# Optimization experiments

Measured on AMD Instinct MI355X. Metric: run time of the kernel, lower is better.

Reference implementation:

```python
import jax, jax.numpy as jnp
import numpy as np

N_NODES = 100000
N_EDGES = 1200000
D_IN = 64
D_HID = 64


def _gcn_layer(h_in, W, b, src, dst, norm, n_nodes):
    # h_in: [N, d_in]; W: [d_in, d_out]; norm: [E_total] symmetric deg norm
    h = h_in @ W                                  # [N, d_out]
    msg = h[src] * norm[:, None]                  # gather + scale, [E_total, d_out]
    agg = jax.ops.segment_sum(msg, dst, num_segments=n_nodes)  # scatter-add
    return agg + b


def _prelu(x, a):
    # per-channel PReLU: a broadcasts over nodes
    return jnp.where(x >= 0, x, a * x)


def setup_inputs() -> dict:
    key = jax.random.key(0)
    ks = jax.random.split(key, 8)
    x = jax.random.normal(ks[0], (N_NODES, D_IN), dtype=jnp.float32)
    edge_index = jax.random.randint(ks[1], (2, N_EDGES), 0, N_NODES, dtype=jnp.int64)
    # Glorot-ish weights, PyG GCNConv defaults: weight + bias; PReLU init slope 0.25
    W1 = jax.random.normal(ks[2], (D_IN, D_HID), dtype=jnp.float32) / np.sqrt(D_IN)
    b1 = jnp.zeros((D_HID,), dtype=jnp.float32)
    a1 = jnp.full((D_HID,), 0.25, dtype=jnp.float32)
    W2 = jax.random.normal(ks[3], (D_HID, D_HID), dtype=jnp.float32) / np.sqrt(D_HID)
    b2 = jnp.zeros((D_HID,), dtype=jnp.float32)
    a2 = jnp.full((D_HID,), 0.25, dtype=jnp.float32)
    return {"x": x, "edge_index": edge_index, "W1": W1, "b1": b1, "a1": a1,
            "W2": W2, "b2": b2, "a2": a2}


def reference(x, edge_index, W1, b1, a1, W2, b2, a2):
    n = x.shape[0]
    # add self-loops (GCNConv default add_self_loops=True)
    loops = jnp.arange(n, dtype=edge_index.dtype)
    src = jnp.concatenate([edge_index[0], loops])
    dst = jnp.concatenate([edge_index[1], loops])
    # symmetric normalization: deg computed on destination with unit edge weights
    deg = jax.ops.segment_sum(jnp.ones_like(src, dtype=x.dtype), dst, num_segments=n)
    dinv = jnp.where(deg > 0, jax.lax.rsqrt(deg), 0.0)
    norm = dinv[src] * dinv[dst]                  # [E + N]

    h = _gcn_layer(x, W1, b1, src, dst, norm, n)
    h = _prelu(h, a1)
    h = _gcn_layer(h, W2, b2, src, dst, norm, n)
    h = _prelu(h, a2)
    return h
```

## Files before the change

### kernel.cpp

```cpp
#include <hip/hip_runtime.h>
#include <hip/hip_bf16.h>
#include <hip/hip_fp16.h>

#define D 64
#define NB 256
#define BSHIFT 8
#define SUBS 8
#define SCAP 1024
#define CHUNK 4096
#define AGN 32
#define BFSTRIDE 16

typedef _Float16 f16x8 __attribute__((ext_vector_type(8)));
typedef float    f32x4 __attribute__((ext_vector_type(4)));


__global__ void __launch_bounds__(256, 4)
k_bin_gemm(const int* __restrict__ src, const int* __restrict__ dst,
           unsigned* __restrict__ records, int* __restrict__ bucket_fill,
           int E, int nbin,
           const float* __restrict__ X, const float* __restrict__ W,
           __half* __restrict__ H, int n, int ntiles, int gemmb) {
    __shared__ int cnt[512];
    __shared__ int gbase[512];
    const int t = threadIdx.x;

    if ((int)blockIdx.x < nbin) {
        const int slot = blockIdx.x & (SUBS - 1);
        cnt[t] = 0; cnt[t + 256] = 0;
        __syncthreads();

        const int base_e = blockIdx.x * CHUNK;
        unsigned rec[16];
        unsigned br[16];
#pragma unroll
        for (int i = 0; i < 16; ++i) {
            int e = base_e + i * 256 + t;
            if (e < E) {
                int s = src[e], d = dst[e];
                int bk = d >> BSHIFT;
                rec[i] = ((unsigned)s << BSHIFT) | (unsigned)(d & (NB - 1));
                int rank = atomicAdd(&cnt[bk], 1);
                br[i] = ((unsigned)bk << 16) | (unsigned)rank;
            } else {
                br[i] = 0xFFFFFFFFu;
            }
        }
        __syncthreads();
#pragma unroll
        for (int rep = 0; rep < 2; ++rep) {
            int bk = t + rep * 256;
            if (cnt[bk] > 0)
                gbase[bk] = atomicAdd(&bucket_fill[(bk * SUBS + slot) * BFSTRIDE], cnt[bk]);
        }
        __syncthreads();
#pragma unroll
        for (int i = 0; i < 16; ++i) {
            if (br[i] != 0xFFFFFFFFu) {
                int bk = br[i] >> 16;
                int idx = gbase[bk] + (int)(br[i] & 0xFFFF);
                if (idx < SCAP)
                    records[((size_t)bk * SUBS + slot) * SCAP + idx] = rec[i];
            }
        }
    } else {
        const int lane = t & 63;
        const int wv   = t >> 6;
        const int r16  = lane & 15;
        const int g4   = lane >> 4;

        f16x8 Bh[4][2], Bl[4][2];
#pragma unroll
        for (int ct = 0; ct < 4; ++ct)
#pragma unroll
            for (int kt = 0; kt < 2; ++kt)
#pragma unroll
                for (int j = 0; j < 8; ++j) {
                    float w = W[(kt * 32 + g4 * 8 + j) * D + ct * 16 + r16];
                    _Float16 h = (_Float16)w;
                    Bh[ct][kt][j] = h;
                    Bl[ct][kt][j] = (_Float16)(w - (float)h);
                }

        const int gw = (blockIdx.x - nbin) * 4 + wv;
        for (int tile = gw; tile < ntiles; tile += gemmb * 4) {
            const int nb16 = tile * 16;
            int row = nb16 + r16;
            if (row > n - 1) row = n - 1;
            const float* xp = X + (size_t)row * D + g4 * 8;
            float4 x0 = *reinterpret_cast<const float4*>(xp);
            float4 x1 = *reinterpret_cast<const float4*>(xp + 4);
            float4 x2 = *reinterpret_cast<const float4*>(xp + 32);
            float4 x3 = *reinterpret_cast<const float4*>(xp + 36);
            float xs[16] = {x0.x, x0.y, x0.z, x0.w, x1.x, x1.y, x1.z, x1.w,
                            x2.x, x2.y, x2.z, x2.w, x3.x, x3.y, x3.z, x3.w};
            f16x8 Ah[2], Al[2];
#pragma unroll
            for (int kt = 0; kt < 2; ++kt)
#pragma unroll
                for (int j = 0; j < 8; ++j) {
                    float v = xs[kt * 8 + j];
                    _Float16 h = (_Float16)v;
                    Ah[kt][j] = h;
                    Al[kt][j] = (_Float16)(v - (float)h);
                }

            f32x4 acc[4];
#pragma unroll
            for (int ct = 0; ct < 4; ++ct)
                acc[ct] = (f32x4){0.f, 0.f, 0.f, 0.f};
#pragma unroll
            for (int ct = 0; ct < 4; ++ct) {
#pragma unroll
                for (int kt = 0; kt < 2; ++kt) {
                    acc[ct] = __builtin_amdgcn_mfma_f32_16x16x32_f16(Ah[kt], Bh[ct][kt], acc[ct], 0, 0, 0);
                    acc[ct] = __builtin_amdgcn_mfma_f32_16x16x32_f16(Al[kt], Bh[ct][kt], acc[ct], 0, 0, 0);
                    acc[ct] = __builtin_amdgcn_mfma_f32_16x16x32_f16(Ah[kt], Bl[ct][kt], acc[ct], 0, 0, 0);
                }
            }
#pragma unroll
            for (int ct = 0; ct < 4; ++ct)
#pragma unroll
                for (int r = 0; r < 4; ++r) {
                    int node = nb16 + g4 * 4 + r;
                    if (node < n)
                        H[(size_t)node * D + ct * 16 + r16] = __float2half_rn(acc[ct][r]);
                }
        }
    }
}


__global__ void k_csr(const unsigned* __restrict__ records,
                      const int* __restrict__ bucket_fill,
                      int* __restrict__ rowptr, float* __restrict__ dinv,
                      int* __restrict__ csr_src, __half* __restrict__ H,
                      int n, int E) {
    __shared__ int bscan[256];
    __shared__ int binc[512];
    __shared__ int cnt[NB];
    __shared__ int excl[NB];
    __shared__ float ddi[NB];
    __shared__ int stage[SUBS * SCAP];

    const int t = threadIdx.x;
    const int b = blockIdx.x;
    const int nbuckets = gridDim.x;

    int s0 = 0, s1 = 0;
#pragma unroll
    for (int s = 0; s < SUBS; ++s) {
        if (2 * t     < nbuckets) s0 += bucket_fill[((2 * t)     * SUBS + s) * BFSTRIDE];
        if (2 * t + 1 < nbuckets) s1 += bucket_fill[((2 * t + 1) * SUBS + s) * BFSTRIDE];
    }
    bscan[t] = s0 + s1;
    __syncthreads();
    for (int off = 1; off < 256; off <<= 1) {
        int val = bscan[t];
        if (t >= off) val += bscan[t - off];
        __syncthreads();
        bscan[t] = val;
        __syncthreads();
    }
    {
        int ep = bscan[t] - (s0 + s1);
        binc[2 * t]     = ep + s0;
        binc[2 * t + 1] = ep + s0 + s1;
    }
    __syncthreads();
    const int base  = (b == 0) ? 0 : binc[b - 1];
    if (b == nbuckets - 1 && t == 0) rowptr[n] = binc[nbuckets - 1];

    int subcnt[SUBS];
    int cnt_e = 0;
#pragma unroll
    for (int s = 0; s < SUBS; ++s) {
        subcnt[s] = bucket_fill[(b * SUBS + s) * BFSTRIDE];
        cnt_e += subcnt[s];
    }

    cnt[t] = 0;
    __syncthreads();
#pragma unroll
    for (int s = 0; s < SUBS; ++s) {
        const size_t so = ((size_t)b * SUBS + s) * SCAP;
        for (int i = t; i < subcnt[s]; i += 256)
            atomicAdd(&cnt[records[so + i] & (NB - 1)], 1);
    }
    __syncthreads();

    const int c0 = cnt[t];
    bscan[t] = c0;
    __syncthreads();
    for (int off = 1; off < 256; off <<= 1) {
        int val = bscan[t];
        if (t >= off) val += bscan[t - off];
        __syncthreads();
        bscan[t] = val;
        __syncthreads();
    }
    excl[t] = bscan[t] - c0;
    {
        int node = b * NB + t;
        float di = rsqrtf((float)(c0 + 1));
        ddi[t] = di;
        if (node < n) {
            rowptr[node] = base + excl[t];
            dinv[node]   = di;
        }
        cnt[t] = 0;
    }
    __syncthreads();

#pragma unroll
    for (int s = 0; s < SUBS; ++s) {
        const size_t so = ((size_t)b * SUBS + s) * SCAP;
        for (int i = t; i < subcnt[s]; i += 256) {
            unsigned r = records[so + i];
            int d8 = r & (NB - 1);
            int rank = atomicAdd(&cnt[d8], 1);
            stage[excl[d8] + rank] = (int)(r >> BSHIFT);
        }
    }
    __syncthreads();

    for (int i = t; i < cnt_e; i += 256)
        csr_src[base + i] = stage[i];

#pragma unroll
    for (int r = 0; r < (NB * 8) / 256; ++r) {
        int idx = r * 256 + t;
        int nl = idx >> 3;
        int node = b * NB + nl;
        if (node < n) {
            int part = (idx & 7) * 8;
            uint4 g = *reinterpret_cast<uint4*>(H + (size_t)node * D + part);
            __half2* p = reinterpret_cast<__half2*>(&g);
            float s = ddi[nl];
#pragma unroll
            for (int i = 0; i < 4; ++i) {
                float2 f = __half22float2(p[i]);
                p[i] = __floats2half2_rn(f.x * s, f.y * s);
            }
            *reinterpret_cast<uint4*>(H + (size_t)node * D + part) = g;
        }
    }
}

__device__ __forceinline__ void edge_accum(const __half* __restrict__ Hn,
                                           const int* __restrict__ csr_src,
                                           int beg, int end, int part, float acc[8]) {
    int idx[8];
#pragma unroll
    for (int j = 0; j < 8; ++j)
        idx[j] = (beg + j < end) ? csr_src[beg + j] : 0;
    int k = beg;
    while (k < end) {
        int s[8];
        float w[8];
#pragma unroll
        for (int j = 0; j < 8; ++j) {
            s[j] = idx[j];
            w[j] = (k + j < end) ? 1.f : 0.f;
        }
        int kn = k + 8;
#pragma unroll
        for (int j = 0; j < 8; ++j)
            idx[j] = (kn + j < end) ? csr_src[kn + j] : 0;
        uint4 g[8];
#pragma unroll
        for (int j = 0; j < 8; ++j)
            g[j] = *reinterpret_cast<const uint4*>(Hn + (size_t)s[j] * D + part);
#pragma unroll
        for (int j = 0; j < 8; ++j) {
            const __half2* p = reinterpret_cast<const __half2*>(&g[j]);
#pragma unroll
            for (int i = 0; i < 4; ++i) {
                float2 f = __half22float2(p[i]);
                acc[2 * i + 0] += w[j] * f.x;
                acc[2 * i + 1] += w[j] * f.y;
            }
        }
        k = kn;
    }
}


__global__ void k_agg_gemm(const __half* __restrict__ Hn1,
                           const int* __restrict__ rowptr,
                           const int* __restrict__ csr_src,
                           const float* __restrict__ dinv,
                           const float* __restrict__ b1, const float* __restrict__ a1,
                           const float* __restrict__ W2,
                           __half* __restrict__ Hn2, int n) {
    __shared__ float W2l[D * D];
    __shared__ float Yl[AGN][68];

    const int t = threadIdx.x;
    for (int i = t; i < (D * D) / 4; i += 256)
        *reinterpret_cast<float4*>(W2l + i * 4) = *reinterpret_cast<const float4*>(W2 + i * 4);

    const int nl   = t >> 3;
    const int part = (t & 7) * 8;
    const int node = blockIdx.x * AGN + nl;

    float di = 0.f;
    if (node < n) {
        di = dinv[node];
        float acc[8];
        {
            uint4 g = *reinterpret_cast<const uint4*>(Hn1 + (size_t)node * D + part);
            const __half2* p = reinterpret_cast<const __half2*>(&g);
#pragma unroll
            for (int i = 0; i < 4; ++i) {
                float2 f = __half22float2(p[i]);
                acc[2 * i + 0] = f.x;
                acc[2 * i + 1] = f.y;
            }
        }
        edge_accum(Hn1, csr_src, rowptr[node], rowptr[node + 1], part, acc);

        const float4 b0 = *reinterpret_cast<const float4*>(b1 + part);
        const float4 b4 = *reinterpret_cast<const float4*>(b1 + part + 4);
        const float4 a0 = *reinterpret_cast<const float4*>(a1 + part);
        const float4 a4 = *reinterpret_cast<const float4*>(a1 + part + 4);
        float y0 = acc[0] * di + b0.x, y1 = acc[1] * di + b0.y;
        float y2 = acc[2] * di + b0.z, y3 = acc[3] * di + b0.w;
        float y4 = acc[4] * di + b4.x, y5 = acc[5] * di + b4.y;
        float y6 = acc[6] * di + b4.z, y7 = acc[7] * di + b4.w;
        Yl[nl][part + 0] = (y0 >= 0.f) ? y0 : a0.x * y0;
        Yl[nl][part + 1] = (y1 >= 0.f) ? y1 : a0.y * y1;
        Yl[nl][part + 2] = (y2 >= 0.f) ? y2 : a0.z * y2;
        Yl[nl][part + 3] = (y3 >= 0.f) ? y3 : a0.w * y3;
        Yl[nl][part + 4] = (y4 >= 0.f) ? y4 : a4.x * y4;
        Yl[nl][part + 5] = (y5 >= 0.f) ? y5 : a4.y * y5;
        Yl[nl][part + 6] = (y6 >= 0.f) ? y6 : a4.z * y6;
        Yl[nl][part + 7] = (y7 >= 0.f) ? y7 : a4.w * y7;
    }
    __syncthreads();

    if (node >= n) return;
    float o[8];
#pragma unroll
    for (int i = 0; i < 8; ++i) o[i] = 0.f;
#pragma unroll 8
    for (int k = 0; k < D; ++k) {
        float yk = Yl[nl][k];
        float4 w0 = *reinterpret_cast<const float4*>(W2l + k * D + part);
        float4 w1 = *reinterpret_cast<const float4*>(W2l + k * D + part + 4);
        o[0] += yk * w0.x; o[1] += yk * w0.y; o[2] += yk * w0.z; o[3] += yk * w0.w;
        o[4] += yk * w1.x; o[5] += yk * w1.y; o[6] += yk * w1.z; o[7] += yk * w1.w;
    }
    __half2 h0 = __floats2half2_rn(o[0] * di, o[1] * di);
    __half2 h1 = __floats2half2_rn(o[2] * di, o[3] * di);
    __half2 h2 = __floats2half2_rn(o[4] * di, o[5] * di);
    __half2 h3 = __floats2half2_rn(o[6] * di, o[7] * di);
    uint4 pack;
    pack.x = *reinterpret_cast<unsigned int*>(&h0);
    pack.y = *reinterpret_cast<unsigned int*>(&h1);
    pack.z = *reinterpret_cast<unsigned int*>(&h2);
    pack.w = *reinterpret_cast<unsigned int*>(&h3);
    *reinterpret_cast<uint4*>(Hn2 + (size_t)node * D + part) = pack;
}


__global__ void k_aggregate(const __half* __restrict__ Hn,
                            const int* __restrict__ rowptr,
                            const int* __restrict__ csr_src,
                            const float* __restrict__ dinv,
                            const float* __restrict__ b, const float* __restrict__ a,
                            float* __restrict__ out, int n) {
    int t = blockIdx.x * blockDim.x + threadIdx.x;
    int node = t >> 3;
    if (node >= n) return;
    int part = (t & 7) * 8;

    float di = dinv[node];
    float acc[8];
    {
        uint4 g = *reinterpret_cast<const uint4*>(Hn + (size_t)node * D + part);
        const __half2* p = reinterpret_cast<const __half2*>(&g);
#pragma unroll
        for (int i = 0; i < 4; ++i) {
            float2 f = __half22float2(p[i]);
            acc[2 * i + 0] = f.x;
            acc[2 * i + 1] = f.y;
        }
    }
    edge_accum(Hn, csr_src, rowptr[node], rowptr[node + 1], part, acc);

    const float4 b0 = *reinterpret_cast<const float4*>(b + part);
    const float4 b4 = *reinterpret_cast<const float4*>(b + part + 4);
    const float4 a0 = *reinterpret_cast<const float4*>(a + part);
    const float4 a4 = *reinterpret_cast<const float4*>(a + part + 4);
    float4 r0, r1;
    r0.x = acc[0] * di + b0.x; r0.y = acc[1] * di + b0.y;
    r0.z = acc[2] * di + b0.z; r0.w = acc[3] * di + b0.w;
    r1.x = acc[4] * di + b4.x; r1.y = acc[5] * di + b4.y;
    r1.z = acc[6] * di + b4.z; r1.w = acc[7] * di + b4.w;
    r0.x = (r0.x >= 0.f) ? r0.x : a0.x * r0.x;
    r0.y = (r0.y >= 0.f) ? r0.y : a0.y * r0.y;
    r0.z = (r0.z >= 0.f) ? r0.z : a0.z * r0.z;
    r0.w = (r0.w >= 0.f) ? r0.w : a0.w * r0.w;
    r1.x = (r1.x >= 0.f) ? r1.x : a4.x * r1.x;
    r1.y = (r1.y >= 0.f) ? r1.y : a4.y * r1.y;
    r1.z = (r1.z >= 0.f) ? r1.z : a4.z * r1.z;
    r1.w = (r1.w >= 0.f) ? r1.w : a4.w * r1.w;
    float* o = out + (size_t)node * D + part;
    *reinterpret_cast<float4*>(o) = r0;
    *reinterpret_cast<float4*>(o + 4) = r1;
}

extern "C" void kernel_launch(void* const* d_in, const int* in_sizes, int n_in,
                              void* d_out, int out_size, void* d_ws, size_t ws_size,
                              hipStream_t stream) {
    const float* x  = (const float*)d_in[0];
    const int*   ei = (const int*)  d_in[1];
    const float* W1 = (const float*)d_in[2];
    const float* b1 = (const float*)d_in[3];
    const float* a1 = (const float*)d_in[4];
    const float* W2 = (const float*)d_in[5];
    const float* b2 = (const float*)d_in[6];
    const float* a2 = (const float*)d_in[7];
    float* out = (float*)d_out;

    const int n   = in_sizes[0] / D;
    const int E   = in_sizes[1] / 2;
    const int n64 = n * D;

    const int* src = ei;
    const int* dst = ei + E;

    const int nbuckets = (n + NB - 1) >> BSHIFT;

    int*      bucket_fill = (int*)d_ws;
    unsigned* records     = (unsigned*)(bucket_fill + 4096 * BFSTRIDE);
    int*      rowptr      = (int*)(records + (size_t)nbuckets * SUBS * SCAP);
    float*    dinv        = (float*)(rowptr + ((n + 257) & ~255));
    int*      csr_src     = (int*)(dinv + ((n + 256) & ~255));
    __half*   Hn1         = (__half*)(csr_src + ((E + 255) & ~255));
    __half*   Hn2         = Hn1 + (((size_t)n64 + 256) & ~(size_t)255);

    const int B = 256;
    const int nbin   = (E + CHUNK - 1) / CHUNK;
    const int gemmb  = 512;
    const int ntiles = (n + 15) / 16;

    hipMemsetAsync(bucket_fill, 0, 4096 * BFSTRIDE * sizeof(int), stream);

    k_bin_gemm<<<nbin + gemmb, B, 0, stream>>>(src, dst, records, bucket_fill, E, nbin,
                                               x, W1, Hn1, n, ntiles, gemmb);
    k_csr<<<nbuckets, B, 0, stream>>>(records, bucket_fill, rowptr, dinv, csr_src,
                                      Hn1, n, E);
    k_agg_gemm<<<(n + AGN - 1) / AGN, B, 0, stream>>>(Hn1, rowptr, csr_src, dinv,
                                                      b1, a1, W2, Hn2, n);
    k_aggregate<<<(n * 8 + B - 1) / B, B, 0, stream>>>(Hn2, rowptr, csr_src, dinv,
                                                       b2, a2, out, n);
}
```

Before: 184.5 us.

## Replace global bucket prefix scan with atomic base allocation and begin/count rows

Each CSR block no longer reads every bucket's fill count and runs a block-wide scan to find its edge offset. Instead it claims its base with one atomicAdd on a global counter, so buckets are laid out in whatever order they finish. Rows are now stored as begin plus count instead of a contiguous rowptr. The per-block scan now uses wavefront shuffles, and the binning loads src/dst as int4. This removes redundant global reads and many barriers, at the cost of a non-deterministic edge layout and an extra per-node array read in the aggregation kernels.

```diff
diff --git a/kernel.cpp b/kernel.cpp
--- a/kernel.cpp
+++ b/kernel.cpp
@@ -5,6 +5,7 @@
 #define D 64
 #define NB 256
 #define BSHIFT 8
+#define NBK 512
 #define SUBS 8
 #define SCAP 1024
 #define CHUNK 4096
@@ -21,8 +22,8 @@
            int E, int nbin,
            const float* __restrict__ X, const float* __restrict__ W,
            __half* __restrict__ H, int n, int ntiles, int gemmb) {
-    __shared__ int cnt[512];
-    __shared__ int gbase[512];
+    __shared__ int cnt[NBK];
+    __shared__ int gbase[NBK];
     const int t = threadIdx.x;
 
     if ((int)blockIdx.x < nbin) {
@@ -34,21 +35,39 @@
         unsigned rec[16];
         unsigned br[16];
 #pragma unroll
-        for (int i = 0; i < 16; ++i) {
-            int e = base_e + i * 256 + t;
-            if (e < E) {
-                int s = src[e], d = dst[e];
-                int bk = d >> BSHIFT;
-                rec[i] = ((unsigned)s << BSHIFT) | (unsigned)(d & (NB - 1));
-                int rank = atomicAdd(&cnt[bk], 1);
-                br[i] = ((unsigned)bk << 16) | (unsigned)rank;
+        for (int i = 0; i < 4; ++i) {
+            const int e0 = base_e + i * 1024 + t * 4;
+            if (e0 + 3 < E) {
+                int4 s4 = *reinterpret_cast<const int4*>(src + e0);
+                int4 d4 = *reinterpret_cast<const int4*>(dst + e0);
+                int ss[4] = {s4.x, s4.y, s4.z, s4.w};
+                int dd[4] = {d4.x, d4.y, d4.z, d4.w};
+#pragma unroll
+                for (int j = 0; j < 4; ++j) {
+                    int bk = dd[j] >> BSHIFT;
+                    rec[i * 4 + j] = ((unsigned)ss[j] << BSHIFT) | (unsigned)(dd[j] & (NB - 1));
+                    int rank = atomicAdd(&cnt[bk], 1);
+                    br[i * 4 + j] = ((unsigned)bk << 16) | (unsigned)rank;
+                }
             } else {
-                br[i] = 0xFFFFFFFFu;
+#pragma unroll
+                for (int j = 0; j < 4; ++j) {
+                    int e = e0 + j;
+                    if (e < E) {
+                        int s = src[e], d = dst[e];
+                        int bk = d >> BSHIFT;
+                        rec[i * 4 + j] = ((unsigned)s << BSHIFT) | (unsigned)(d & (NB - 1));
+                        int rank = atomicAdd(&cnt[bk], 1);
+                        br[i * 4 + j] = ((unsigned)bk << 16) | (unsigned)rank;
+                    } else {
+                        br[i * 4 + j] = 0xFFFFFFFFu;
+                    }
+                }
             }
         }
         __syncthreads();
 #pragma unroll
-        for (int rep = 0; rep < 2; ++rep) {
+        for (int rep = 0; rep < NBK / 256; ++rep) {
             int bk = t + rep * 256;
             if (cnt[bk] > 0)
                 gbase[bk] = atomicAdd(&bucket_fill[(bk * SUBS + slot) * BFSTRIDE], cnt[bk]);
@@ -133,43 +152,20 @@
 
 __global__ void k_csr(const unsigned* __restrict__ records,
                       const int* __restrict__ bucket_fill,
-                      int* __restrict__ rowptr, float* __restrict__ dinv,
-                      int* __restrict__ csr_src, __half* __restrict__ H,
-                      int n, int E) {
-    __shared__ int bscan[256];
-    __shared__ int binc[512];
+                      int* __restrict__ edge_base,
+                      int* __restrict__ rowbeg, int* __restrict__ rowcnt,
+                      float* __restrict__ dinv,
+                      int* __restrict__ csr_src, __half* __restrict__ H, int n) {
     __shared__ int cnt[NB];
     __shared__ int excl[NB];
     __shared__ float ddi[NB];
+    __shared__ int wsum[4];
+    __shared__ int sbase;
     __shared__ int stage[SUBS * SCAP];
 
     const int t = threadIdx.x;
     const int b = blockIdx.x;
-    const int nbuckets = gridDim.x;
-
-    int s0 = 0, s1 = 0;
-#pragma unroll
-    for (int s = 0; s < SUBS; ++s) {
-        if (2 * t     < nbuckets) s0 += bucket_fill[((2 * t)     * SUBS + s) * BFSTRIDE];
-        if (2 * t + 1 < nbuckets) s1 += bucket_fill[((2 * t + 1) * SUBS + s) * BFSTRIDE];
-    }
-    bscan[t] = s0 + s1;
-    __syncthreads();
-    for (int off = 1; off < 256; off <<= 1) {
-        int val = bscan[t];
-        if (t >= off) val += bscan[t - off];
-        __syncthreads();
-        bscan[t] = val;
-        __syncthreads();
-    }
-    {
-        int ep = bscan[t] - (s0 + s1);
-        binc[2 * t]     = ep + s0;
-        binc[2 * t + 1] = ep + s0 + s1;
-    }
-    __syncthreads();
-    const int base  = (b == 0) ? 0 : binc[b - 1];
-    if (b == nbuckets - 1 && t == 0) rowptr[n] = binc[nbuckets - 1];
+    const int lane = t & 63;
 
     int subcnt[SUBS];
     int cnt_e = 0;
@@ -190,26 +186,33 @@
     __syncthreads();
 
     const int c0 = cnt[t];
-    bscan[t] = c0;
-    __syncthreads();
-    for (int off = 1; off < 256; off <<= 1) {
-        int val = bscan[t];
-        if (t >= off) val += bscan[t - off];
-        __syncthreads();
-        bscan[t] = val;
-        __syncthreads();
-    }
-    excl[t] = bscan[t] - c0;
+    int v = c0;
+#pragma unroll
+    for (int off = 1; off < 64; off <<= 1) {
+        int u = __shfl_up(v, off, 64);
+        if (lane >= off) v += u;
+    }
+    if (lane == 63) wsum[t >> 6] = v;
+    if (t == 0) sbase = atomicAdd(edge_base, cnt_e);
+    __syncthreads();
+    int pre = 0;
+#pragma unroll
+    for (int w = 0; w < 4; ++w)
+        if (w < (t >> 6)) pre += wsum[w];
+    const int ex = v + pre - c0;
+    excl[t] = ex;
+    const int base = sbase;
+    float di = rsqrtf((float)(c0 + 1));
+    ddi[t] = di;
     {
         int node = b * NB + t;
-        float di = rsqrtf((float)(c0 + 1));
-        ddi[t] = di;
         if (node < n) {
-            rowptr[node] = base + excl[t];
+            rowbeg[node] = base + ex;
+            rowcnt[node] = c0;
             dinv[node]   = di;
         }
-        cnt[t] = 0;
-    }
+    }
+    cnt[t] = 0;
     __syncthreads();
 
 #pragma unroll
@@ -287,7 +290,8 @@
 
 
 __global__ void k_agg_gemm(const __half* __restrict__ Hn1,
-                           const int* __restrict__ rowptr,
+                           const int* __restrict__ rowbeg,
+                           const int* __restrict__ rowcnt,
                            const int* __restrict__ csr_src,
                            const float* __restrict__ dinv,
                            const float* __restrict__ b1, const float* __restrict__ a1,
@@ -318,7 +322,8 @@
                 acc[2 * i + 1] = f.y;
             }
         }
-        edge_accum(Hn1, csr_src, rowptr[node], rowptr[node + 1], part, acc);
+        const int beg = rowbeg[node];
+        edge_accum(Hn1, csr_src, beg, beg + rowcnt[node], part, acc);
 
         const float4 b0 = *reinterpret_cast<const float4*>(b1 + part);
         const float4 b4 = *reinterpret_cast<const float4*>(b1 + part + 4);
@@ -365,7 +370,8 @@
 
 
 __global__ void k_aggregate(const __half* __restrict__ Hn,
-                            const int* __restrict__ rowptr,
+                            const int* __restrict__ rowbeg,
+                            const int* __restrict__ rowcnt,
                             const int* __restrict__ csr_src,
                             const float* __restrict__ dinv,
                             const float* __restrict__ b, const float* __restrict__ a,
@@ -387,7 +393,8 @@
             acc[2 * i + 1] = f.y;
         }
     }
-    edge_accum(Hn, csr_src, rowptr[node], rowptr[node + 1], part, acc);
+    const int beg = rowbeg[node];
+    edge_accum(Hn, csr_src, beg, beg + rowcnt[node], part, acc);
 
     const float4 b0 = *reinterpret_cast<const float4*>(b + part);
     const float4 b4 = *reinterpret_cast<const float4*>(b + part + 4);
@@ -434,9 +441,11 @@
     const int nbuckets = (n + NB - 1) >> BSHIFT;
 
     int*      bucket_fill = (int*)d_ws;
+    int*      edge_base   = bucket_fill + 60000;
     unsigned* records     = (unsigned*)(bucket_fill + 4096 * BFSTRIDE);
-    int*      rowptr      = (int*)(records + (size_t)nbuckets * SUBS * SCAP);
-    float*    dinv        = (float*)(rowptr + ((n + 257) & ~255));
+    int*      rowbeg      = (int*)(records + (size_t)nbuckets * SUBS * SCAP);
+    int*      rowcnt      = rowbeg + ((n + 256) & ~255);
+    float*    dinv        = (float*)(rowcnt + ((n + 256) & ~255));
     int*      csr_src     = (int*)(dinv + ((n + 256) & ~255));
     __half*   Hn1         = (__half*)(csr_src + ((E + 255) & ~255));
     __half*   Hn2         = Hn1 + (((size_t)n64 + 256) & ~(size_t)255);
@@ -450,10 +459,10 @@
 
     k_bin_gemm<<<nbin + gemmb, B, 0, stream>>>(src, dst, records, bucket_fill, E, nbin,
                                                x, W1, Hn1, n, ntiles, gemmb);
-    k_csr<<<nbuckets, B, 0, stream>>>(records, bucket_fill, rowptr, dinv, csr_src,
-                                      Hn1, n, E);
-    k_agg_gemm<<<(n + AGN - 1) / AGN, B, 0, stream>>>(Hn1, rowptr, csr_src, dinv,
+    k_csr<<<nbuckets, B, 0, stream>>>(records, bucket_fill, edge_base,
+                                      rowbeg, rowcnt, dinv, csr_src, Hn1, n);
+    k_agg_gemm<<<(n + AGN - 1) / AGN, B, 0, stream>>>(Hn1, rowbeg, rowcnt, csr_src, dinv,
                                                       b1, a1, W2, Hn2, n);
-    k_aggregate<<<(n * 8 + B - 1) / B, B, 0, stream>>>(Hn2, rowptr, csr_src, dinv,
+    k_aggregate<<<(n * 8 + B - 1) / B, B, 0, stream>>>(Hn2, rowbeg, rowcnt, csr_src, dinv,
                                                        b2, a2, out, n);
 }
```

New measurement: 182.7 us. No clear change (-1.0%).
